# Performance work log

Hardware: AMD Instinct MI355X
Metric: run time of the kernel (lower is better)

## Reference

```python
import jax, jax.numpy as jnp
import numpy as np

N_HEADS = 16

def _rel_emb(table, len_q, len_k):
    # table: [2P+1, d] -> [len_q, len_k, d] via clipped relative distance lookup
    P = (table.shape[0] - 1) // 2
    rel = jnp.arange(len_k)[None, :] - jnp.arange(len_q)[:, None]
    idx = jnp.clip(rel, -P, P) + P
    return table[idx]

def setup_inputs() -> dict:
    key = jax.random.key(0)
    ks = jax.random.split(key, 13)
    B, S, E = 2, 2048, 1024
    P = 128
    d = E // N_HEADS
    s = 0.02
    return {
        "q": jax.random.normal(ks[0], (B, S, E), jnp.float32),
        "k": jax.random.normal(ks[1], (B, S, E), jnp.float32),
        "v": jax.random.normal(ks[2], (B, S, E), jnp.float32),
        "Wq": jax.random.normal(ks[3], (E, E), jnp.float32) * s,
        "bq": jnp.zeros((E,), jnp.float32),
        "Wk": jax.random.normal(ks[4], (E, E), jnp.float32) * s,
        "bk": jnp.zeros((E,), jnp.float32),
        "Wv": jax.random.normal(ks[5], (E, E), jnp.float32) * s,
        "bv": jnp.zeros((E,), jnp.float32),
        "Wo": jax.random.normal(ks[6], (E, E), jnp.float32) * s,
        "bo": jnp.zeros((E,), jnp.float32),
        "rk_table": jax.random.normal(ks[7], (2 * P + 1, d), jnp.float32) * s,
        "rv_table": jax.random.normal(ks[8], (2 * P + 1, d), jnp.float32) * s,
    }

def reference(q, k, v, Wq, bq, Wk, bk, Wv, bv, Wo, bo, rk_table, rv_table):
    B, Sq, E = q.shape
    Sk = k.shape[1]
    H = N_HEADS
    d = E // H
    scale = jnp.sqrt(jnp.asarray(d, q.dtype))

    qh = (q @ Wq.T + bq).reshape(B, Sq, H, d).transpose(0, 2, 1, 3)  # [B,H,Sq,d]
    kh = (k @ Wk.T + bk).reshape(B, Sk, H, d).transpose(0, 2, 1, 3)
    vh = (v @ Wv.T + bv).reshape(B, Sk, H, d).transpose(0, 2, 1, 3)

    qk = jnp.einsum('bhqd,bhkd->bhqk', qh, kh)
    r_k = _rel_emb(rk_table, Sq, Sk)                 # [Sq,Sk,d]
    q_rk = jnp.einsum('bhqd,qkd->bhqk', qh, r_k)
    attn = jax.nn.softmax((qk + q_rk) / scale, axis=-1)  # dropout p=0

    w1 = jnp.einsum('bhqk,bhkd->bhqd', attn, vh)
    r_v = _rel_emb(rv_table, Sq, Sk)
    w2 = jnp.einsum('bhqk,qkd->bhqd', attn, r_v)

    out = (w1 + w2).transpose(0, 2, 1, 3).reshape(B, Sq, E)
    return out @ Wo.T + bo
```

## Files before the change

kernel.cpp:

```cpp
#include <hip/hip_runtime.h>
#include <hip/hip_bf16.h>
#include <cstdint>
#include <cstddef>

#define NH   16
#define DH   64
#define SQ   2048
#define NB   2
#define EM   1024
#define NREL 257
#define QSTR 258
#define SCL  0.18033688f

typedef unsigned short ushort_t;
using bf16x8 = __attribute__((ext_vector_type(8))) __bf16;
using bf16x4 = __attribute__((ext_vector_type(4))) __bf16;
using f32x4  = __attribute__((ext_vector_type(4))) float;
#define MFMA16(a, b, c) __builtin_amdgcn_mfma_f32_16x16x32_bf16(a, b, c, 0, 0, 0)

__device__ __forceinline__ ushort_t f2bf(float f) {
    union { __bf16 h; ushort_t u; } x; x.h = (__bf16)f; return x.u;
}
__device__ __forceinline__ float bf2f(ushort_t u) {
    union { unsigned u; float f; } x; x.u = ((unsigned)u) << 16;
    return x.f;
}
__device__ __forceinline__ uint2 pack4(float a, float b, float c, float d) {
    union { bf16x4 v; uint2 u; } x;
    x.v = (bf16x4){ (__bf16)a, (__bf16)b, (__bf16)c, (__bf16)d };
    return x.u;
}
__device__ __forceinline__ int kperm(int x) {
    return (x & ~63) | ((x & 15) << 2) | ((x >> 4) & 3);
}

__global__ __launch_bounds__(256)
void cvt3(const float* __restrict__ a, const float* __restrict__ b,
          const float* __restrict__ c, ushort_t* __restrict__ oa,
          ushort_t* __restrict__ ob, ushort_t* __restrict__ oc, int n)
{
    const float* in = blockIdx.y == 0 ? a : (blockIdx.y == 1 ? b : c);
    ushort_t* out   = blockIdx.y == 0 ? oa : (blockIdx.y == 1 ? ob : oc);
    int i = (blockIdx.x * 256 + threadIdx.x) * 8;
    if (i < n) {
        float4 v0 = *reinterpret_cast<const float4*>(in + i);
        float4 v1 = *reinterpret_cast<const float4*>(in + i + 4);
        uint2 lo = pack4(v0.x, v0.y, v0.z, v0.w);
        uint2 hi = pack4(v1.x, v1.y, v1.z, v1.w);
        *reinterpret_cast<uint4*>(out + i) = make_uint4(lo.x, lo.y, hi.x, hi.y);
    }
}
__global__ __launch_bounds__(256)
void cvt4(const float* __restrict__ a, const float* __restrict__ b,
          const float* __restrict__ c, const float* __restrict__ d,
          ushort_t* __restrict__ oa, ushort_t* __restrict__ ob,
          ushort_t* __restrict__ oc, ushort_t* __restrict__ od, int n)
{
    const float* in = blockIdx.y == 0 ? a : (blockIdx.y == 1 ? b :
                      (blockIdx.y == 2 ? c : d));
    ushort_t* out   = blockIdx.y == 0 ? oa : (blockIdx.y == 1 ? ob :
                      (blockIdx.y == 2 ? oc : od));
    int i = (blockIdx.x * 256 + threadIdx.x) * 8;
    if (i < n) {
        float4 v0 = *reinterpret_cast<const float4*>(in + i);
        float4 v1 = *reinterpret_cast<const float4*>(in + i + 4);
        uint2 lo = pack4(v0.x, v0.y, v0.z, v0.w);
        uint2 hi = pack4(v1.x, v1.y, v1.z, v1.w);
        *reinterpret_cast<uint4*>(out + i) = make_uint4(lo.x, lo.y, hi.x, hi.y);
    }
}

__global__ __launch_bounds__(256)
void prep_tables(const float* __restrict__ rv, const float* __restrict__ rk,
                 ushort_t* __restrict__ rvT, ushort_t* __restrict__ rkb)
{
    int idx = blockIdx.x * 256 + threadIdx.x;
    if (idx < 64 * 256) {
        int d = idx >> 8, c = idx & 255;
        rvT[d * 256 + kperm(c)] = f2bf(rv[(size_t)(c + 1) * DH + d]);
    }
    idx -= 64 * 256;
    if (idx >= 0 && idx < 272 * 64) {
        int j = idx >> 6, d2 = idx & 63;
        rkb[idx] = (j < NREL) ? f2bf(rk[(size_t)j * DH + d2]) : (ushort_t)0;
    }
}

template<int MODE>
__global__ __launch_bounds__(256)
void gemm_bt(const ushort_t* __restrict__ A, const ushort_t* __restrict__ W,
             const float* __restrict__ bias, void* __restrict__ dstv,
             int M, int N, int K)
{
    __shared__ ushort_t As[128 * 40];
    __shared__ ushort_t Bs[128 * 40];
    const int t = threadIdx.x, lane = t & 63;
    const int wv = t >> 6, wr = wv >> 1, wc = wv & 1;
    const int g = lane >> 4, c16 = lane & 15;

    const int nwg = gridDim.x * gridDim.y;
    int flat = blockIdx.y * gridDim.x + blockIdx.x;
    int rm = (flat & 7) * (nwg >> 3) + (flat >> 3);
    const int n0 = (rm % gridDim.x) * 128;
    const int m0 = (rm / gridDim.x) * 128;

    f32x4 acc[4][4];
#pragma unroll
    for (int i = 0; i < 4; ++i)
#pragma unroll
        for (int j = 0; j < 4; ++j) acc[i][j] = (f32x4){0.f, 0.f, 0.f, 0.f};

    for (int k0 = 0; k0 < K; k0 += 32) {
        __syncthreads();
#pragma unroll
        for (int l = 0; l < 2; ++l) {
            const int fid = t + 256 * l;
            const int row = fid >> 2, ch = fid & 3;
            uint4 av = *reinterpret_cast<const uint4*>(A + (size_t)(m0 + row) * K + k0 + ch * 8);
            uint4 wv4 = *reinterpret_cast<const uint4*>(W + (size_t)(n0 + row) * K + k0 + ch * 8);
            *reinterpret_cast<uint4*>(As + row * 40 + ch * 8) = av;
            *reinterpret_cast<uint4*>(Bs + row * 40 + ch * 8) = wv4;
        }
        __syncthreads();

        bf16x8 af[4], bfr[4];
#pragma unroll
        for (int i = 0; i < 4; ++i)
            af[i] = *reinterpret_cast<const bf16x8*>(As + (wr * 64 + i * 16 + c16) * 40 + g * 8);
#pragma unroll
        for (int j = 0; j < 4; ++j)
            bfr[j] = *reinterpret_cast<const bf16x8*>(Bs + (wc * 64 + j * 16 + c16) * 40 + g * 8);
#pragma unroll
        for (int i = 0; i < 4; ++i)
#pragma unroll
            for (int j = 0; j < 4; ++j)
                acc[i][j] = MFMA16(af[i], bfr[j], acc[i][j]);
    }

#pragma unroll
    for (int j = 0; j < 4; ++j) {
        const int n = n0 + wc * 64 + j * 16 + c16;
        const float bn = bias[n];
#pragma unroll
        for (int i = 0; i < 4; ++i) {
#pragma unroll
            for (int r = 0; r < 4; ++r) {
                const int m = m0 + wr * 64 + i * 16 + 4 * g + r;
                const float vv = acc[i][j][r] + bn;
                if (MODE == 0) {
                    ((float*)dstv)[(size_t)m * N + n] = vv;
                } else {
                    const int b = m >> 11, s = m & (SQ - 1);
                    const int h = n >> 6, dd = n & 63;
                    if (MODE == 1) {
                        ((ushort_t*)dstv)[(((size_t)b * NH + h) * SQ + s) * DH + dd] = f2bf(vv);
                    } else {
                        const int sp = kperm(s);
                        ((ushort_t*)dstv)[(((size_t)b * NH + h) * DH + dd) * SQ + sp] = f2bf(vv);
                    }
                }
            }
        }
    }
}

__global__ __launch_bounds__(256)
void qrel_mfma(const ushort_t* __restrict__ qh, const ushort_t* __restrict__ rkb,
               ushort_t* __restrict__ qrel)
{
    const int t = threadIdx.x, lane = t & 63, w = t >> 6;
    const int g = lane >> 4, c16 = lane & 15;
    const size_t r0 = (size_t)blockIdx.x * 64 + w * 16;

    bf16x8 af[2];
#pragma unroll
    for (int ks = 0; ks < 2; ++ks)
        af[ks] = *reinterpret_cast<const bf16x8*>(qh + (r0 + c16) * DH + ks * 32 + g * 8);

    f32x4 acc[17];
#pragma unroll
    for (int n = 0; n < 17; ++n) acc[n] = (f32x4){0.f, 0.f, 0.f, 0.f};
#pragma unroll
    for (int n = 0; n < 17; ++n)
#pragma unroll
        for (int ks = 0; ks < 2; ++ks) {
            bf16x8 bf = *reinterpret_cast<const bf16x8*>(
                rkb + (size_t)(16 * n + c16) * DH + ks * 32 + g * 8);
            acc[n] = MFMA16(af[ks], bf, acc[n]);
        }
#pragma unroll
    for (int n = 0; n < 17; ++n) {
        const int j = 16 * n + c16;
        if (j < NREL) {
#pragma unroll
            for (int r = 0; r < 4; ++r)
                qrel[(r0 + 4 * g + r) * QSTR + j] = f2bf(acc[n][r] * SCL);
        }
    }
}

__global__ __launch_bounds__(256, 4)
void attn_flash(const ushort_t* __restrict__ qh, const ushort_t* __restrict__ kh,
                const ushort_t* __restrict__ vt, const ushort_t* __restrict__ qrel,
                ushort_t* __restrict__ Ptile, float* __restrict__ w1g,
                float* __restrict__ lacg, float* __restrict__ b0g,
                float* __restrict__ b256g)
{
    __shared__ ushort_t Ks[64 * 72];
    __shared__ ushort_t Vs[64 * 72];
    __shared__ ushort_t PQs[64 * 72];

    const int t = threadIdx.x, lane = t & 63, w = t >> 6;
    const int g = lane >> 4, c16 = lane & 15;
    const int nwg = gridDim.x * gridDim.y;
    int flat = blockIdx.y * gridDim.x + blockIdx.x;
    int rmid = (flat & 7) * (nwg >> 3) + (flat >> 3);
    const int q0 = (rmid & 31) * 64;
    const int bh = rmid >> 5;
    const size_t Gbase = ((size_t)bh * 32 + (q0 >> 6)) * 5;

#pragma unroll
    for (int l = 0; l < 2; ++l) {
        const int fid = t + 256 * l;
        const int row = fid >> 3, ch = fid & 7;
        uint4 v = *reinterpret_cast<const uint4*>(
            qh + ((size_t)bh * SQ + q0 + row) * DH + ch * 8);
        *reinterpret_cast<uint4*>(PQs + row * 72 + ch * 8) = v;
    }
    __syncthreads();
    bf16x8 qf[2];
#pragma unroll
    for (int ks = 0; ks < 2; ++ks)
        qf[ks] = *reinterpret_cast<const bf16x8*>(PQs + (w * 16 + c16) * 72 + ks * 32 + g * 8);

    float q0add[4], q256add[4];
#pragma unroll
    for (int i = 0; i < 4; ++i) {
        const size_t r = (size_t)bh * SQ + q0 + w * 16 + 4 * g + i;
        q0add[i]   = bf2f(qrel[r * QSTR + 0]);
        q256add[i] = bf2f(qrel[r * QSTR + 256]);
    }

    f32x4 w1[4];
#pragma unroll
    for (int n = 0; n < 4; ++n) w1[n] = (f32x4){0.f, 0.f, 0.f, 0.f};
    float lac[4] = {0.f,0.f,0.f,0.f}, b0[4] = {0.f,0.f,0.f,0.f}, b256[4] = {0.f,0.f,0.f,0.f};

    const int row_l = t >> 3, ch_l = t & 7;
    const int row_h = row_l + 32;
    uint4 kr0, kr1, vr0, vr1;
    {
        kr0 = *reinterpret_cast<const uint4*>(kh + ((size_t)bh * SQ + row_l) * DH + ch_l * 8);
        kr1 = *reinterpret_cast<const uint4*>(kh + ((size_t)bh * SQ + row_h) * DH + ch_l * 8);
        vr0 = *reinterpret_cast<const uint4*>(vt + ((size_t)bh * DH + row_l) * SQ + ch_l * 8);
        vr1 = *reinterpret_cast<const uint4*>(vt + ((size_t)bh * DH + row_h) * SQ + ch_l * 8);
    }

    for (int k0 = 0; k0 < SQ; k0 += 64) {
        __syncthreads();
        *reinterpret_cast<uint4*>(Ks + row_l * 72 + ch_l * 8) = kr0;
        *reinterpret_cast<uint4*>(Ks + row_h * 72 + ch_l * 8) = kr1;
        *reinterpret_cast<uint4*>(Vs + row_l * 72 + ch_l * 8) = vr0;
        *reinterpret_cast<uint4*>(Vs + row_h * 72 + ch_l * 8) = vr1;
        __syncthreads();
        if (k0 + 64 < SQ) {
            kr0 = *reinterpret_cast<const uint4*>(kh + ((size_t)bh * SQ + k0 + 64 + row_l) * DH + ch_l * 8);
            kr1 = *reinterpret_cast<const uint4*>(kh + ((size_t)bh * SQ + k0 + 64 + row_h) * DH + ch_l * 8);
            vr0 = *reinterpret_cast<const uint4*>(vt + ((size_t)bh * DH + row_l) * SQ + k0 + 64 + ch_l * 8);
            vr1 = *reinterpret_cast<const uint4*>(vt + ((size_t)bh * DH + row_h) * SQ + k0 + 64 + ch_l * 8);
        }

        f32x4 s[4];
#pragma unroll
        for (int n = 0; n < 4; ++n) s[n] = (f32x4){0.f, 0.f, 0.f, 0.f};
        __builtin_amdgcn_s_setprio(1);
#pragma unroll
        for (int ks = 0; ks < 2; ++ks)
#pragma unroll
            for (int n = 0; n < 4; ++n) {
                bf16x8 kf = *reinterpret_cast<const bf16x8*>(
                    Ks + (16 * n + c16) * 72 + ks * 32 + g * 8);
                s[n] = MFMA16(qf[ks], kf, s[n]);
            }
        __builtin_amdgcn_s_setprio(0);

        const int rel0 = k0 - q0;
        float rsum[4] = {0.f, 0.f, 0.f, 0.f};
        if (rel0 <= -192 || rel0 >= 192) {
            const bool lo = rel0 < 0;
#pragma unroll
            for (int i = 0; i < 4; ++i) {
                const float add = lo ? q0add[i] : q256add[i];
#pragma unroll
                for (int n = 0; n < 4; ++n) {
                    const float p = exp2f(fmaf(s[n][i], SCL, add));
                    s[n][i] = p; rsum[i] += p;
                }
                if (lo) b0[i] += rsum[i]; else b256[i] += rsum[i];
                *reinterpret_cast<uint2*>(PQs + (w * 16 + 4 * g + i) * 72 + c16 * 4) =
                    pack4(s[0][i], s[1][i], s[2][i], s[3][i]);
            }
        } else if (rel0 == -128 || rel0 == 128) {
            const int tix = (rel0 >> 6) + 2;
#pragma unroll
            for (int i = 0; i < 4; ++i) {
                const int qloc = w * 16 + 4 * g + i;
                const int qg = q0 + qloc;
                const ushort_t* qrow = qrel + ((size_t)bh * SQ + qg) * QSTR;
                float z[4];
#pragma unroll
                for (int n = 0; n < 4; ++n) {
                    const int rel = (k0 + 16 * n + c16) - qg;
                    const int idx = rel < -128 ? 0 : (rel > 128 ? 256 : rel + 128);
                    const float p = exp2f(fmaf(s[n][i], SCL, bf2f(qrow[idx])));
                    s[n][i] = p; rsum[i] += p;
                    const bool inb = (rel >= -127) & (rel <= 127);
                    z[n] = inb ? p : 0.f;
                    if (rel <= -128)      b0[i] += p;
                    else if (rel >= 128)  b256[i] += p;
                }
                *reinterpret_cast<uint2*>(PQs + qloc * 72 + c16 * 4) =
                    pack4(s[0][i], s[1][i], s[2][i], s[3][i]);
                *reinterpret_cast<uint2*>(
                    Ptile + ((Gbase + tix) * 64 + qloc) * 64 + 4 * c16) =
                    pack4(z[0], z[1], z[2], z[3]);
            }
        } else {
            const int tix = (rel0 >> 6) + 2;
#pragma unroll
            for (int i = 0; i < 4; ++i) {
                const int qloc = w * 16 + 4 * g + i;
                const int qg = q0 + qloc;
                const ushort_t* qrow = qrel + ((size_t)bh * SQ + qg) * QSTR;
#pragma unroll
                for (int n = 0; n < 4; ++n) {
                    const int rel = (k0 + 16 * n + c16) - qg;
                    const float p = exp2f(fmaf(s[n][i], SCL, bf2f(qrow[rel + 128])));
                    s[n][i] = p; rsum[i] += p;
                }
                const uint2 pk = pack4(s[0][i], s[1][i], s[2][i], s[3][i]);
                *reinterpret_cast<uint2*>(PQs + qloc * 72 + c16 * 4) = pk;
                *reinterpret_cast<uint2*>(
                    Ptile + ((Gbase + tix) * 64 + qloc) * 64 + 4 * c16) = pk;
            }
        }
#pragma unroll
        for (int i = 0; i < 4; ++i) lac[i] += rsum[i];

        __builtin_amdgcn_s_setprio(1);
#pragma unroll
        for (int ks = 0; ks < 2; ++ks) {
            bf16x8 pf = *reinterpret_cast<const bf16x8*>(
                PQs + (w * 16 + c16) * 72 + ks * 32 + g * 8);
#pragma unroll
            for (int n = 0; n < 4; ++n) {
                bf16x8 vf = *reinterpret_cast<const bf16x8*>(
                    Vs + (16 * n + c16) * 72 + ks * 32 + g * 8);
                w1[n] = MFMA16(pf, vf, w1[n]);
            }
        }
        __builtin_amdgcn_s_setprio(0);
    }

#pragma unroll
    for (int m = 1; m < 16; m <<= 1)
#pragma unroll
        for (int i = 0; i < 4; ++i) {
            lac[i]  += __shfl_xor(lac[i],  m, 64);
            b0[i]   += __shfl_xor(b0[i],   m, 64);
            b256[i] += __shfl_xor(b256[i], m, 64);
        }
    if (c16 == 0) {
#pragma unroll
        for (int i = 0; i < 4; ++i) {
            const size_t row = (size_t)bh * SQ + q0 + w * 16 + 4 * g + i;
            lacg[row] = lac[i]; b0g[row] = b0[i]; b256g[row] = b256[i];
        }
    }
#pragma unroll
    for (int n = 0; n < 4; ++n)
#pragma unroll
        for (int i = 0; i < 4; ++i) {
            const size_t row = (size_t)bh * SQ + q0 + w * 16 + 4 * g + i;
            w1g[row * DH + 16 * n + c16] = w1[n][i];
        }
}

__global__ __launch_bounds__(256)
void band_gemm(const ushort_t* __restrict__ Ptile, const ushort_t* __restrict__ rvT,
               const float* __restrict__ rv_f32, const float* __restrict__ w1g,
               const float* __restrict__ lacg, const float* __restrict__ b0g,
               const float* __restrict__ b256g, ushort_t* __restrict__ wout)
{
    __shared__ ushort_t Pband[64 * 264];
    const int t = threadIdx.x, lane = t & 63, w = t >> 6;
    const int g = lane >> 4, c16 = lane & 15;
    const int G = blockIdx.x;
    const size_t r0 = (size_t)G * 64;
    const int q0 = (G & 31) * 64;

    for (int i = t; i < 64 * 264 / 2; i += 256)
        reinterpret_cast<unsigned*>(Pband)[i] = 0u;
    __syncthreads();

    for (int u = t; u < 5 * 64 * 16; u += 256) {
        const int tix = u >> 10;
        const int kt0 = q0 + (tix - 2) * 64;
        if (kt0 < 0 || kt0 >= SQ) continue;
        const int qloc = (u >> 4) & 63;
        const int c = u & 15;
        uint2 pv = *reinterpret_cast<const uint2*>(
            Ptile + (((size_t)G * 5 + tix) * 64 + qloc) * 64 + 4 * c);
        const ushort_t* pe = reinterpret_cast<const ushort_t*>(&pv);
        const int relbase = (tix - 2) * 64 - qloc + 127;
#pragma unroll
        for (int n = 0; n < 4; ++n) {
            const int x = relbase + 16 * n + c;
            if (x >= 0 && x <= 254)
                Pband[qloc * 264 + ((x & ~63) | ((x & 15) << 2) | ((x >> 4) & 3))] = pe[n];
        }
    }
    if (t < 64) Pband[t * 264 + 255] = f2bf(b256g[r0 + t]);
    __syncthreads();

    f32x4 acc[4];
#pragma unroll
    for (int n = 0; n < 4; ++n) acc[n] = (f32x4){0.f, 0.f, 0.f, 0.f};
#pragma unroll
    for (int ks = 0; ks < 8; ++ks) {
        bf16x8 pm = *reinterpret_cast<const bf16x8*>(
            Pband + (w * 16 + c16) * 264 + ks * 32 + g * 8);
#pragma unroll
        for (int n = 0; n < 4; ++n) {
            bf16x8 rf = *reinterpret_cast<const bf16x8*>(
                rvT + (size_t)(16 * n + c16) * 256 + ks * 32 + g * 8);
            acc[n] = MFMA16(pm, rf, acc[n]);
        }
    }

#pragma unroll
    for (int i = 0; i < 4; ++i) {
        const size_t row = r0 + w * 16 + 4 * g + i;
        const float inv = 1.0f / lacg[row];
        const float vb0 = b0g[row];
        const int b = (int)(row >> 15), h = (int)((row >> 11) & 15), s = (int)(row & 2047);
#pragma unroll
        for (int n = 0; n < 4; ++n) {
            const int col = 16 * n + c16;
            const float val = (w1g[row * DH + col] + acc[n][i] + vb0 * rv_f32[col]) * inv;
            wout[(((size_t)b * SQ + s) * NH + h) * DH + col] = f2bf(val);
        }
    }
}

extern "C" void kernel_launch(void* const* d_in, const int* in_sizes, int n_in,
                              void* d_out, int out_size, void* d_ws, size_t ws_size,
                              hipStream_t stream)
{
    const float* q  = (const float*)d_in[0];
    const float* k  = (const float*)d_in[1];
    const float* v  = (const float*)d_in[2];
    const float* Wq = (const float*)d_in[3];
    const float* bq = (const float*)d_in[4];
    const float* Wk = (const float*)d_in[5];
    const float* bk = (const float*)d_in[6];
    const float* Wv = (const float*)d_in[7];
    const float* bv = (const float*)d_in[8];
    const float* Wo = (const float*)d_in[9];
    const float* bo = (const float*)d_in[10];
    const float* rk = (const float*)d_in[11];
    const float* rv = (const float*)d_in[12];

    char* ws = (char*)d_ws;
    auto alloc = [&](size_t bytes) { char* p = ws; ws += bytes; return p; };
    const size_t QB = (size_t)NB * SQ * EM * 2;
    const size_t WB = (size_t)EM * EM * 2;
    const size_t NR = (size_t)NB * NH * SQ;

    char* region0 = alloc(NR * 320 * 2);
    ushort_t* Ptile = (ushort_t*)region0;
    ushort_t* qbf = (ushort_t*)region0;
    ushort_t* kbf = (ushort_t*)(region0 + QB);
    ushort_t* vbf = (ushort_t*)(region0 + 2 * QB);
    ushort_t* Wqb = (ushort_t*)(region0 + 3 * QB);
    ushort_t* Wkb = (ushort_t*)(region0 + 3 * QB + WB);
    ushort_t* Wvb = (ushort_t*)(region0 + 3 * QB + 2 * WB);

    ushort_t* Wob  = (ushort_t*)alloc(WB);
    ushort_t* qhb  = (ushort_t*)alloc(QB);
    ushort_t* khb  = (ushort_t*)alloc(QB);
    ushort_t* vtb  = (ushort_t*)alloc(QB);
    ushort_t* wbuf = (ushort_t*)alloc(QB);
    ushort_t* rvT  = (ushort_t*)alloc(64 * 256 * 2);
    ushort_t* rkb  = (ushort_t*)alloc(272 * 64 * 2);
    ushort_t* qrel = (ushort_t*)alloc(NR * QSTR * 2);
    float*    w1g  = (float*)alloc(NR * DH * 4);
    float*    lacg = (float*)alloc(NR * 4);
    float*    b0g  = (float*)alloc(NR * 4);
    float*    b256g= (float*)alloc(NR * 4);

    const int NQ = NB * SQ * EM;
    const int NW = EM * EM;
    cvt3<<<dim3(NQ / 2048, 3), 256, 0, stream>>>(q, k, v, qbf, kbf, vbf, NQ);
    cvt4<<<dim3(NW / 2048, 4), 256, 0, stream>>>(Wq, Wk, Wv, Wo, Wqb, Wkb, Wvb, Wob, NW);
    prep_tables<<<132, 256, 0, stream>>>(rv, rk, rvT, rkb);

    const int M = NB * SQ;
    dim3 gg(EM / 128, M / 128);
    gemm_bt<1><<<gg, 256, 0, stream>>>(qbf, Wqb, bq, qhb, M, EM, EM);
    gemm_bt<1><<<gg, 256, 0, stream>>>(kbf, Wkb, bk, khb, M, EM, EM);
    gemm_bt<2><<<gg, 256, 0, stream>>>(vbf, Wvb, bv, vtb, M, EM, EM);
    qrel_mfma<<<(int)(NR / 64), 256, 0, stream>>>(qhb, rkb, qrel);

    attn_flash<<<dim3(32, 32), 256, 0, stream>>>(qhb, khb, vtb, qrel,
                                                 Ptile, w1g, lacg, b0g, b256g);
    band_gemm<<<(int)(NR / 64), 256, 0, stream>>>(Ptile, rvT, rv, w1g, lacg,
                                                  b0g, b256g, wbuf);
    gemm_bt<0><<<gg, 256, 0, stream>>>(wbuf, Wob, bo, d_out, M, EM, EM);
}
```

Measured before the change: 279.8 us.

## Double-buffer K/V tiles in LDS with XOR swizzle and one barrier per step

Turns the attention kernel's K/V shared-memory staging into a double buffer, so the next tile is written to the alternate buffer after the PV MFMAs. This removes one of the two barriers per key step. It replaces the padded 72-stride LDS layout with a 64-stride XOR-swizzled layout to avoid bank conflicts, and batches the fragment loads ahead of the MFMA chains. It also hardcodes the grid remap constant. LDS use grows, from three 64x72 tiles to five 64x64 tiles, which could reduce occupancy under the 4-block launch bound.

```diff
diff --git a/kernel.cpp b/kernel.cpp
--- a/kernel.cpp
+++ b/kernel.cpp
@@ -11,6 +11,7 @@
 #define NREL 257
 #define QSTR 258
 #define SCL  0.18033688f
+#define NR   ((size_t)NB * NH * SQ)
 
 typedef unsigned short ushort_t;
 using bf16x8 = __attribute__((ext_vector_type(8))) __bf16;
@@ -32,6 +33,9 @@
 }
 __device__ __forceinline__ int kperm(int x) {
     return (x & ~63) | ((x & 15) << 2) | ((x >> 4) & 3);
+}
+__device__ __forceinline__ int lswz(int row, int byteoff) {
+    return row * 128 + (byteoff ^ ((row & 7) << 4));
 }
 
 __global__ __launch_bounds__(256)
@@ -206,18 +210,23 @@
                 float* __restrict__ lacg, float* __restrict__ b0g,
                 float* __restrict__ b256g)
 {
-    __shared__ ushort_t Ks[64 * 72];
-    __shared__ ushort_t Vs[64 * 72];
-    __shared__ ushort_t PQs[64 * 72];
+    __shared__ ushort_t Ks[2][64 * 64];
+    __shared__ ushort_t Vs[2][64 * 64];
+    __shared__ ushort_t PQs[64 * 64];
+    char* Ksb = (char*)Ks; char* Vsb = (char*)Vs; char* PQb = (char*)PQs;
 
     const int t = threadIdx.x, lane = t & 63, w = t >> 6;
     const int g = lane >> 4, c16 = lane & 15;
-    const int nwg = gridDim.x * gridDim.y;
     int flat = blockIdx.y * gridDim.x + blockIdx.x;
-    int rmid = (flat & 7) * (nwg >> 3) + (flat >> 3);
+    int rmid = (flat & 7) * 128 + (flat >> 3);
     const int q0 = (rmid & 31) * 64;
     const int bh = rmid >> 5;
-    const size_t Gbase = ((size_t)bh * 32 + (q0 >> 6)) * 5;
+    const size_t Gbase = (size_t)rmid * 5;
+
+    const ushort_t* kp = kh + (size_t)bh * SQ * DH;
+    const ushort_t* vp = vt + (size_t)bh * DH * SQ;
+    const int row_l = t >> 3, ch_l = t & 7;
+    const int row_h = row_l + 32;
 
 #pragma unroll
     for (int l = 0; l < 2; ++l) {
@@ -225,20 +234,36 @@
         const int row = fid >> 3, ch = fid & 7;
         uint4 v = *reinterpret_cast<const uint4*>(
             qh + ((size_t)bh * SQ + q0 + row) * DH + ch * 8);
-        *reinterpret_cast<uint4*>(PQs + row * 72 + ch * 8) = v;
-    }
+        *reinterpret_cast<uint4*>(PQb + lswz(row, ch * 16)) = v;
+    }
+    uint4 kr0, kr1, vr0, vr1;
+    kr0 = *reinterpret_cast<const uint4*>(kp + (size_t)row_l * DH + ch_l * 8);
+    kr1 = *reinterpret_cast<const uint4*>(kp + (size_t)row_h * DH + ch_l * 8);
+    vr0 = *reinterpret_cast<const uint4*>(vp + (size_t)row_l * SQ + ch_l * 8);
+    vr1 = *reinterpret_cast<const uint4*>(vp + (size_t)row_h * SQ + ch_l * 8);
     __syncthreads();
     bf16x8 qf[2];
 #pragma unroll
     for (int ks = 0; ks < 2; ++ks)
-        qf[ks] = *reinterpret_cast<const bf16x8*>(PQs + (w * 16 + c16) * 72 + ks * 32 + g * 8);
-
+        qf[ks] = *reinterpret_cast<const bf16x8*>(
+            PQb + lswz(w * 16 + c16, ks * 64 + g * 16));
+
+    *reinterpret_cast<uint4*>(Ksb + lswz(row_l, ch_l * 16)) = kr0;
+    *reinterpret_cast<uint4*>(Ksb + lswz(row_h, ch_l * 16)) = kr1;
+    *reinterpret_cast<uint4*>(Vsb + lswz(row_l, ch_l * 16)) = vr0;
+    *reinterpret_cast<uint4*>(Vsb + lswz(row_h, ch_l * 16)) = vr1;
+    kr0 = *reinterpret_cast<const uint4*>(kp + (size_t)(64 + row_l) * DH + ch_l * 8);
+    kr1 = *reinterpret_cast<const uint4*>(kp + (size_t)(64 + row_h) * DH + ch_l * 8);
+    vr0 = *reinterpret_cast<const uint4*>(vp + (size_t)row_l * SQ + 64 + ch_l * 8);
+    vr1 = *reinterpret_cast<const uint4*>(vp + (size_t)row_h * SQ + 64 + ch_l * 8);
+
+    const ushort_t* qrb = qrel + ((size_t)bh * SQ + q0) * QSTR;
     float q0add[4], q256add[4];
 #pragma unroll
     for (int i = 0; i < 4; ++i) {
-        const size_t r = (size_t)bh * SQ + q0 + w * 16 + 4 * g + i;
-        q0add[i]   = bf2f(qrel[r * QSTR + 0]);
-        q256add[i] = bf2f(qrel[r * QSTR + 256]);
+        const int r = w * 16 + 4 * g + i;
+        q0add[i]   = bf2f(qrb[(size_t)r * QSTR + 0]);
+        q256add[i] = bf2f(qrb[(size_t)r * QSTR + 256]);
     }
 
     f32x4 w1[4];
@@ -246,43 +271,31 @@
     for (int n = 0; n < 4; ++n) w1[n] = (f32x4){0.f, 0.f, 0.f, 0.f};
     float lac[4] = {0.f,0.f,0.f,0.f}, b0[4] = {0.f,0.f,0.f,0.f}, b256[4] = {0.f,0.f,0.f,0.f};
 
-    const int row_l = t >> 3, ch_l = t & 7;
-    const int row_h = row_l + 32;
-    uint4 kr0, kr1, vr0, vr1;
-    {
-        kr0 = *reinterpret_cast<const uint4*>(kh + ((size_t)bh * SQ + row_l) * DH + ch_l * 8);
-        kr1 = *reinterpret_cast<const uint4*>(kh + ((size_t)bh * SQ + row_h) * DH + ch_l * 8);
-        vr0 = *reinterpret_cast<const uint4*>(vt + ((size_t)bh * DH + row_l) * SQ + ch_l * 8);
-        vr1 = *reinterpret_cast<const uint4*>(vt + ((size_t)bh * DH + row_h) * SQ + ch_l * 8);
-    }
+    __syncthreads();
+    int cur = 0;
 
     for (int k0 = 0; k0 < SQ; k0 += 64) {
-        __syncthreads();
-        *reinterpret_cast<uint4*>(Ks + row_l * 72 + ch_l * 8) = kr0;
-        *reinterpret_cast<uint4*>(Ks + row_h * 72 + ch_l * 8) = kr1;
-        *reinterpret_cast<uint4*>(Vs + row_l * 72 + ch_l * 8) = vr0;
-        *reinterpret_cast<uint4*>(Vs + row_h * 72 + ch_l * 8) = vr1;
-        __syncthreads();
-        if (k0 + 64 < SQ) {
-            kr0 = *reinterpret_cast<const uint4*>(kh + ((size_t)bh * SQ + k0 + 64 + row_l) * DH + ch_l * 8);
-            kr1 = *reinterpret_cast<const uint4*>(kh + ((size_t)bh * SQ + k0 + 64 + row_h) * DH + ch_l * 8);
-            vr0 = *reinterpret_cast<const uint4*>(vt + ((size_t)bh * DH + row_l) * SQ + k0 + 64 + ch_l * 8);
-            vr1 = *reinterpret_cast<const uint4*>(vt + ((size_t)bh * DH + row_h) * SQ + k0 + 64 + ch_l * 8);
-        }
+        const int co = cur * 8192;
 
         f32x4 s[4];
 #pragma unroll
         for (int n = 0; n < 4; ++n) s[n] = (f32x4){0.f, 0.f, 0.f, 0.f};
-        __builtin_amdgcn_s_setprio(1);
-#pragma unroll
-        for (int ks = 0; ks < 2; ++ks)
-#pragma unroll
-            for (int n = 0; n < 4; ++n) {
-                bf16x8 kf = *reinterpret_cast<const bf16x8*>(
-                    Ks + (16 * n + c16) * 72 + ks * 32 + g * 8);
-                s[n] = MFMA16(qf[ks], kf, s[n]);
-            }
-        __builtin_amdgcn_s_setprio(0);
+        {
+            bf16x8 kf[4][2];
+#pragma unroll
+            for (int n = 0; n < 4; ++n)
+#pragma unroll
+                for (int ks = 0; ks < 2; ++ks)
+                    kf[n][ks] = *reinterpret_cast<const bf16x8*>(
+                        Ksb + co + lswz(16 * n + c16, ks * 64 + g * 16));
+            __builtin_amdgcn_s_setprio(1);
+#pragma unroll
+            for (int ks = 0; ks < 2; ++ks)
+#pragma unroll
+                for (int n = 0; n < 4; ++n)
+                    s[n] = MFMA16(qf[ks], kf[n][ks], s[n]);
+            __builtin_amdgcn_s_setprio(0);
+        }
 
         const int rel0 = k0 - q0;
         float rsum[4] = {0.f, 0.f, 0.f, 0.f};
@@ -297,20 +310,20 @@
                     s[n][i] = p; rsum[i] += p;
                 }
                 if (lo) b0[i] += rsum[i]; else b256[i] += rsum[i];
-                *reinterpret_cast<uint2*>(PQs + (w * 16 + 4 * g + i) * 72 + c16 * 4) =
+                const int qloc = w * 16 + 4 * g + i;
+                *reinterpret_cast<uint2*>(PQb + lswz(qloc, c16 * 8)) =
                     pack4(s[0][i], s[1][i], s[2][i], s[3][i]);
             }
         } else if (rel0 == -128 || rel0 == 128) {
-            const int tix = (rel0 >> 6) + 2;
+            const int tix = (rel0 + 128) >> 6;
 #pragma unroll
             for (int i = 0; i < 4; ++i) {
                 const int qloc = w * 16 + 4 * g + i;
-                const int qg = q0 + qloc;
-                const ushort_t* qrow = qrel + ((size_t)bh * SQ + qg) * QSTR;
+                const ushort_t* qrow = qrb + (size_t)qloc * QSTR;
                 float z[4];
 #pragma unroll
                 for (int n = 0; n < 4; ++n) {
-                    const int rel = (k0 + 16 * n + c16) - qg;
+                    const int rel = rel0 + 16 * n + c16 - qloc;
                     const int idx = rel < -128 ? 0 : (rel > 128 ? 256 : rel + 128);
                     const float p = exp2f(fmaf(s[n][i], SCL, bf2f(qrow[idx])));
                     s[n][i] = p; rsum[i] += p;
@@ -319,27 +332,26 @@
                     if (rel <= -128)      b0[i] += p;
                     else if (rel >= 128)  b256[i] += p;
                 }
-                *reinterpret_cast<uint2*>(PQs + qloc * 72 + c16 * 4) =
+                *reinterpret_cast<uint2*>(PQb + lswz(qloc, c16 * 8)) =
                     pack4(s[0][i], s[1][i], s[2][i], s[3][i]);
                 *reinterpret_cast<uint2*>(
                     Ptile + ((Gbase + tix) * 64 + qloc) * 64 + 4 * c16) =
                     pack4(z[0], z[1], z[2], z[3]);
             }
         } else {
-            const int tix = (rel0 >> 6) + 2;
+            const int tix = (rel0 + 128) >> 6;
 #pragma unroll
             for (int i = 0; i < 4; ++i) {
                 const int qloc = w * 16 + 4 * g + i;
-                const int qg = q0 + qloc;
-                const ushort_t* qrow = qrel + ((size_t)bh * SQ + qg) * QSTR;
+                const ushort_t* qrow = qrb + (size_t)qloc * QSTR;
 #pragma unroll
                 for (int n = 0; n < 4; ++n) {
-                    const int rel = (k0 + 16 * n + c16) - qg;
+                    const int rel = rel0 + 16 * n + c16 - qloc;
                     const float p = exp2f(fmaf(s[n][i], SCL, bf2f(qrow[rel + 128])));
                     s[n][i] = p; rsum[i] += p;
                 }
                 const uint2 pk = pack4(s[0][i], s[1][i], s[2][i], s[3][i]);
-                *reinterpret_cast<uint2*>(PQs + qloc * 72 + c16 * 4) = pk;
+                *reinterpret_cast<uint2*>(PQb + lswz(qloc, c16 * 8)) = pk;
                 *reinterpret_cast<uint2*>(
                     Ptile + ((Gbase + tix) * 64 + qloc) * 64 + 4 * c16) = pk;
             }
@@ -347,19 +359,43 @@
 #pragma unroll
         for (int i = 0; i < 4; ++i) lac[i] += rsum[i];
 
-        __builtin_amdgcn_s_setprio(1);
-#pragma unroll
-        for (int ks = 0; ks < 2; ++ks) {
-            bf16x8 pf = *reinterpret_cast<const bf16x8*>(
-                PQs + (w * 16 + c16) * 72 + ks * 32 + g * 8);
-#pragma unroll
-            for (int n = 0; n < 4; ++n) {
-                bf16x8 vf = *reinterpret_cast<const bf16x8*>(
-                    Vs + (16 * n + c16) * 72 + ks * 32 + g * 8);
-                w1[n] = MFMA16(pf, vf, w1[n]);
+        {
+            bf16x8 vf[4][2];
+#pragma unroll
+            for (int n = 0; n < 4; ++n)
+#pragma unroll
+                for (int ks = 0; ks < 2; ++ks)
+                    vf[n][ks] = *reinterpret_cast<const bf16x8*>(
+                        Vsb + co + lswz(16 * n + c16, ks * 64 + g * 16));
+            bf16x8 pf[2];
+#pragma unroll
+            for (int ks = 0; ks < 2; ++ks)
+                pf[ks] = *reinterpret_cast<const bf16x8*>(
+                    PQb + lswz(w * 16 + c16, ks * 64 + g * 16));
+            __builtin_amdgcn_s_setprio(1);
+#pragma unroll
+            for (int ks = 0; ks < 2; ++ks)
+#pragma unroll
+                for (int n = 0; n < 4; ++n)
+                    w1[n] = MFMA16(pf[ks], vf[n][ks], w1[n]);
+            __builtin_amdgcn_s_setprio(0);
+        }
+
+        if (k0 + 64 < SQ) {
+            const int cn = (cur ^ 1) * 8192;
+            *reinterpret_cast<uint4*>(Ksb + cn + lswz(row_l, ch_l * 16)) = kr0;
+            *reinterpret_cast<uint4*>(Ksb + cn + lswz(row_h, ch_l * 16)) = kr1;
+            *reinterpret_cast<uint4*>(Vsb + cn + lswz(row_l, ch_l * 16)) = vr0;
+            *reinterpret_cast<uint4*>(Vsb + cn + lswz(row_h, ch_l * 16)) = vr1;
+            if (k0 + 128 < SQ) {
+                kr0 = *reinterpret_cast<const uint4*>(kp + (size_t)(k0 + 128 + row_l) * DH + ch_l * 8);
+                kr1 = *reinterpret_cast<const uint4*>(kp + (size_t)(k0 + 128 + row_h) * DH + ch_l * 8);
+                vr0 = *reinterpret_cast<const uint4*>(vp + (size_t)row_l * SQ + k0 + 128 + ch_l * 8);
+                vr1 = *reinterpret_cast<const uint4*>(vp + (size_t)row_h * SQ + k0 + 128 + ch_l * 8);
             }
         }
-        __builtin_amdgcn_s_setprio(0);
+        __syncthreads();
+        cur ^= 1;
     }
 
 #pragma unroll
@@ -475,7 +511,6 @@
     auto alloc = [&](size_t bytes) { char* p = ws; ws += bytes; return p; };
     const size_t QB = (size_t)NB * SQ * EM * 2;
     const size_t WB = (size_t)EM * EM * 2;
-    const size_t NR = (size_t)NB * NH * SQ;
 
     char* region0 = alloc(NR * 320 * 2);
     ushort_t* Ptile = (ushort_t*)region0;
```

Result: slower. 325.8 us (+16.5%).
